# Kernel tuning notes

Hardware: AMD Instinct MI355X
Metric: run time of the kernel (lower is better)

## Reference

```python
import jax, jax.numpy as jnp
import numpy as np


def setup_inputs() -> dict:
    key = jax.random.key(0)
    k1, k2, k3 = jax.random.split(key, 3)
    N, E, D_IN, D_OUT = 100000, 1600000, 64, 64
    x = jax.random.normal(k1, (N, D_IN), dtype=jnp.float32)
    edge_index = jax.random.randint(k2, (2, E), 0, N, dtype=jnp.int64)
    # Glorot-style init for the GCN weight, zero bias (PyG defaults)
    W = jax.random.normal(k3, (D_IN, D_OUT), dtype=jnp.float32) * (1.0 / np.sqrt(D_IN))
    b = jnp.zeros((D_OUT,), dtype=jnp.float32)
    return {"x": x, "edge_index": edge_index, "W": W, "b": b}


def reference(x, edge_index, W, b):
    # GCNConv (PyG semantics, add_self_loops=True, normalize=True) followed by
    # Dropout (eval mode -> identity) and ReLU.
    N = x.shape[0]
    # Linear transform first (small GEMM)
    xw = x @ W  # [N, D_OUT]
    # Add self-loops
    loops = jnp.arange(N, dtype=edge_index.dtype)
    row = jnp.concatenate([edge_index[0], loops])  # source nodes
    col = jnp.concatenate([edge_index[1], loops])  # destination nodes
    # Symmetric degree normalization: deg over destination index (PyG gcn_norm)
    ones = jnp.ones(col.shape[0], dtype=xw.dtype)
    deg = jax.ops.segment_sum(ones, col, num_segments=N)
    deg_inv_sqrt = jnp.where(deg > 0, jax.lax.rsqrt(deg), 0.0)
    norm = deg_inv_sqrt[row] * deg_inv_sqrt[col]  # [E+N]
    # Gather source features, scale, scatter-add to destinations
    msgs = norm[:, None] * xw[row]  # [E+N, D_OUT]
    out = jax.ops.segment_sum(msgs, col, num_segments=N)
    out = out + b
    # dropout in eval mode is identity
    return jax.nn.relu(out)
```

## Files before the change

kernel.cpp:

```cpp
#include <hip/hip_runtime.h>
#include <hip/hip_fp16.h>


#define D 64
#define BW 256
#define CAPB 4800
#define CAPL 6912
#define EPT 16
#define PART_T 512
#define EPB (PART_T * EPT)
#define NBMAX 512
#define GSTRIDE 16

typedef __attribute__((ext_vector_type(8))) short bf16x8;
typedef __attribute__((ext_vector_type(4))) float f32x4;

__device__ __forceinline__ unsigned short f2bf(float f) {
    unsigned u = __float_as_uint(f);
    u += 0x7FFFu + ((u >> 16) & 1u);
    return (unsigned short)(u >> 16);
}

__global__ __launch_bounds__(512)
void k_part(const int* __restrict__ row, const int* __restrict__ col,
            int* __restrict__ gcur, int* __restrict__ dense,
            unsigned short* __restrict__ WT, const float* __restrict__ W,
            unsigned short* __restrict__ xw_h,
            int E, int NBUCK, int N) {
    __shared__ int lh[NBMAX];
    __shared__ int lst[NBMAX + 1];
    __shared__ int bas[NBMAX];
    __shared__ int wsc[8];
    __shared__ int srtv[EPB];
    int tid = threadIdx.x;
    for (int i = tid; i < NBUCK; i += PART_T) lh[i] = 0;
    __syncthreads();
    int e0 = blockIdx.x * EPB + tid;
    int rr[EPT], cc[EPT], pp[EPT];
#pragma unroll
    for (int i = 0; i < EPT; ++i) {
        int e = e0 + i * PART_T;
        if (e < E) {
            cc[i] = __builtin_nontemporal_load(col + e);
            rr[i] = __builtin_nontemporal_load(row + e);
            pp[i] = atomicAdd(&lh[cc[i] >> 8], 1);
        } else {
            cc[i] = -1;
        }
    }
    __syncthreads();
    int rot = (int)((blockIdx.x * 97u) % (unsigned)NBUCK);
    for (int j = tid; j < NBUCK; j += PART_T) {
        int bu = j + rot; if (bu >= NBUCK) bu -= NBUCK;
        int h = lh[bu];
        if (h > 0) bas[bu] = atomicAdd(&gcur[bu * GSTRIDE], h);
    }
    int lane = tid & 63, wv = tid >> 6;
    int v = (tid < NBUCK) ? lh[tid] : 0;
    int inc = v;
#pragma unroll
    for (int o = 1; o < 64; o <<= 1) {
        int u = __shfl_up(inc, o);
        if (lane >= o) inc += u;
    }
    if (lane == 63) wsc[wv] = inc;
    __syncthreads();
    int woff = 0;
#pragma unroll
    for (int w = 0; w < 8; ++w) woff += (w < wv) ? wsc[w] : 0;
    if (tid < NBUCK) lst[tid] = woff + inc - v;
    int tot = min(EPB, E - blockIdx.x * EPB);
    if (tid == 0) lst[NBUCK] = tot;
    __syncthreads();
#pragma unroll
    for (int i = 0; i < EPT; ++i) {
        if (cc[i] >= 0)
            srtv[lst[cc[i] >> 8] + pp[i]] = (rr[i] << 8) | (cc[i] & 255);
    }
    __syncthreads();
    for (int p = tid; p < tot; p += PART_T) {
        int lo = 0, hi = NBUCK;
        while (hi - lo > 1) {
            int mid = (lo + hi) >> 1;
            if (lst[mid] <= p) lo = mid; else hi = mid;
        }
        int gpos = bas[lo] + (p - lst[lo]);
        if (gpos < CAPB) dense[(size_t)lo * CAPB + gpos] = srtv[p];
    }
    if (blockIdx.x == 0) {
        for (int i = tid; i < 4096; i += PART_T) {
            int n = i >> 6, k = i & 63;
            WT[i] = f2bf(W[k * 64 + n]);
        }
        if (tid < 32) ((unsigned*)xw_h)[(size_t)N * 32 + tid] = 0u;
    }
}

__global__ __launch_bounds__(256, 4)
void k_gemm(const float* __restrict__ x, const unsigned short* __restrict__ WT,
            const int* __restrict__ dense, const int* __restrict__ gcur,
            unsigned char* __restrict__ deg8, unsigned short* __restrict__ xw_h,
            int N, int NT) {
    __shared__ int lh[BW];
    int tid = threadIdx.x, b = blockIdx.x;
    lh[tid] = 0;
    __syncthreads();
    int tot = min(gcur[b * GSTRIDE], CAPB);
    const int* dn = dense + (size_t)b * CAPB;
    for (int i = tid; i < tot; i += 256)
        atomicAdd(&lh[__builtin_nontemporal_load(dn + i) & 255], 1);
    __syncthreads();
    {
        int node = b * BW + tid;
        if (node < N) deg8[node] = (unsigned char)min(lh[tid], 255);
    }
    int lane = tid & 63, wv = tid >> 6;
    int m = lane & 15, quad = lane >> 4;
    bf16x8 Bf[4][2];
#pragma unroll
    for (int t = 0; t < 4; ++t)
#pragma unroll
        for (int s = 0; s < 2; ++s)
            Bf[t][s] = *(const bf16x8*)(WT + (t * 16 + m) * 64 + s * 32 + quad * 8);
#pragma unroll
    for (int s = 0; s < 4; ++s) {
        int mt = b * 16 + s * 4 + wv;
        if (mt >= NT) continue;
        int row0 = mt * 16;
        const float* xr = x + (size_t)(row0 + m) * 64 + quad * 8;
        f32x4 a0 = __builtin_nontemporal_load((const f32x4*)(xr));
        f32x4 a1 = __builtin_nontemporal_load((const f32x4*)(xr + 4));
        f32x4 a2 = __builtin_nontemporal_load((const f32x4*)(xr + 32));
        f32x4 a3 = __builtin_nontemporal_load((const f32x4*)(xr + 36));
        bf16x8 A0, A1;
        A0[0] = (short)f2bf(a0[0]); A0[1] = (short)f2bf(a0[1]);
        A0[2] = (short)f2bf(a0[2]); A0[3] = (short)f2bf(a0[3]);
        A0[4] = (short)f2bf(a1[0]); A0[5] = (short)f2bf(a1[1]);
        A0[6] = (short)f2bf(a1[2]); A0[7] = (short)f2bf(a1[3]);
        A1[0] = (short)f2bf(a2[0]); A1[1] = (short)f2bf(a2[1]);
        A1[2] = (short)f2bf(a2[2]); A1[3] = (short)f2bf(a2[3]);
        A1[4] = (short)f2bf(a3[0]); A1[5] = (short)f2bf(a3[1]);
        A1[6] = (short)f2bf(a3[2]); A1[7] = (short)f2bf(a3[3]);
        f32x4 acc[4];
#pragma unroll
        for (int t = 0; t < 4; ++t) {
            acc[t] = (f32x4){0.f, 0.f, 0.f, 0.f};
            acc[t] = __builtin_amdgcn_mfma_f32_16x16x32_bf16(Bf[t][0], A0, acc[t], 0, 0, 0);
            acc[t] = __builtin_amdgcn_mfma_f32_16x16x32_bf16(Bf[t][1], A1, acc[t], 0, 0, 0);
        }
        float dsc = rsqrtf((float)(lh[(row0 + m) & 255] + 1));
        unsigned short* op = xw_h + (size_t)(row0 + m) * 64 + quad * 4;
#pragma unroll
        for (int t = 0; t < 4; ++t) {
            __half2 h0, h1;
            h0.x = __float2half(acc[t][0] * dsc); h0.y = __float2half(acc[t][1] * dsc);
            h1.x = __float2half(acc[t][2] * dsc); h1.y = __float2half(acc[t][3] * dsc);
            uint2 u; u.x = *(unsigned*)&h0; u.y = *(unsigned*)&h1;
            *(uint2*)(op + t * 16) = u;
        }
    }
}

__global__ __launch_bounds__(1024, 8)
void k_gather(const int* __restrict__ dense, const int* __restrict__ gcur,
              const unsigned char* __restrict__ deg8,
              const uint2* __restrict__ xwh, const float* __restrict__ bias,
              float* __restrict__ out, int N) {
    __shared__ int lh[BW], stt[BW], cur[BW];
    __shared__ int wsum[4];
    __shared__ __align__(16) int srtL[CAPL];
    int b = blockIdx.x, tid = threadIdx.x, lane = tid & 63;
    int v = 0, vp = 0, inc = 0;
    if (tid < BW) {
        int node = b * BW + tid;
        v = (node < N) ? (int)deg8[node] : 0;
        lh[tid] = v;
        vp = (v + 15) & ~15; inc = vp;
#pragma unroll
        for (int o = 1; o < 64; o <<= 1) {
            int u = __shfl_up(inc, o);
            if (lane >= o) inc += u;
        }
        if (lane == 63) wsum[tid >> 6] = inc;
    }
    __syncthreads();
    if (tid < BW) {
        int wv4 = tid >> 6, woff = 0;
#pragma unroll
        for (int w = 0; w < 4; ++w) woff += (w < wv4) ? wsum[w] : 0;
        int st = woff + inc - vp;
        stt[tid] = st;
        cur[tid] = st;
    }
    __syncthreads();
    int tot = min(gcur[b * GSTRIDE], CAPB);
    const int* dn = dense + (size_t)b * CAPB;
    for (int i = tid; i < tot; i += 1024) {
        int val = __builtin_nontemporal_load(dn + i);
        int pos = atomicAdd(&cur[val & 255], 1);
        if (pos < CAPL) srtL[pos] = val >> 8;
    }
    __syncthreads();
    if (tid < BW) {
        int e = stt[tid] + v, ep = min(stt[tid] + vp, CAPL);
        for (; e < ep; ++e) srtL[e] = N;
    }
    __syncthreads();
    int q = lane >> 4;
    int l = lane & 15;
    int wv = tid >> 6;
    const float4 bb = ((const float4*)bias)[l];
#define ADDV(h)                                                     \
    {                                                               \
        __half2 h0 = *(__half2*)&(h).x, h1 = *(__half2*)&(h).y;     \
        float2 f0 = __half22float2(h0), f1 = __half22float2(h1);    \
        acc.x += f0.x; acc.y += f0.y; acc.z += f1.x; acc.w += f1.y; \
    }
    for (int nn = wv * 16; nn < wv * 16 + 16; ++nn) {
        int node = b * BW + nn;
        if (node >= N) break;
        int k = lh[nn], s0 = stt[nn];
        int kp = (k + 15) & ~15;
        if (s0 + kp > CAPL) kp = (CAPL > s0) ? ((CAPL - s0) & ~15) : 0;
        float4 acc = make_float4(0.f, 0.f, 0.f, 0.f);
        if (q == 0) { uint2 hs = xwh[(size_t)node * 16 + l]; ADDV(hs); }
        int rounds = kp >> 4;
        if (rounds > 0) {
            int i0 = s0 + q;
            int r0 = srtL[i0], r1 = srtL[i0 + 4], r2 = srtL[i0 + 8], r3 = srtL[i0 + 12];
            uint2 va = xwh[(size_t)r0 * 16 + l];
            uint2 vb = xwh[(size_t)r1 * 16 + l];
            uint2 vc = xwh[(size_t)r2 * 16 + l];
            uint2 vd = xwh[(size_t)r3 * 16 + l];
            for (int r = 1; r < rounds; ++r) {
                i0 += 16;
                int s0n = srtL[i0], s1n = srtL[i0 + 4], s2n = srtL[i0 + 8], s3n = srtL[i0 + 12];
                uint2 wa = xwh[(size_t)s0n * 16 + l];
                uint2 wb = xwh[(size_t)s1n * 16 + l];
                uint2 wc = xwh[(size_t)s2n * 16 + l];
                uint2 wd = xwh[(size_t)s3n * 16 + l];
                ADDV(va); ADDV(vb); ADDV(vc); ADDV(vd);
                va = wa; vb = wb; vc = wc; vd = wd;
            }
            ADDV(va); ADDV(vb); ADDV(vc); ADDV(vd);
        }
        acc.x += __shfl_xor(acc.x, 16); acc.y += __shfl_xor(acc.y, 16);
        acc.z += __shfl_xor(acc.z, 16); acc.w += __shfl_xor(acc.w, 16);
        acc.x += __shfl_xor(acc.x, 32); acc.y += __shfl_xor(acc.y, 32);
        acc.z += __shfl_xor(acc.z, 32); acc.w += __shfl_xor(acc.w, 32);
        if (q == 0) {
            float dn2 = rsqrtf((float)(k + 1));
            f32x4 o;
            o[0] = fmaxf(fmaf(dn2, acc.x, bb.x), 0.f);
            o[1] = fmaxf(fmaf(dn2, acc.y, bb.y), 0.f);
            o[2] = fmaxf(fmaf(dn2, acc.z, bb.z), 0.f);
            o[3] = fmaxf(fmaf(dn2, acc.w, bb.w), 0.f);
            __builtin_nontemporal_store(o, (f32x4*)(out + ((size_t)node * 16 + l) * 4));
        }
    }
#undef ADDV
}

extern "C" void kernel_launch(void* const* d_in, const int* in_sizes, int n_in,
                              void* d_out, int out_size, void* d_ws, size_t ws_size,
                              hipStream_t stream) {
    const float* x    = (const float*)d_in[0];
    const int*   ei   = (const int*)d_in[1];
    const float* W    = (const float*)d_in[2];
    const float* bias = (const float*)d_in[3];
    float* out = (float*)d_out;

    const int N = in_sizes[0] / D;
    const int E = in_sizes[1] / 2;
    const int* row = ei;
    const int* col = ei + E;

    const int NBUCK = (N + BW - 1) / BW;
    const int NB1   = (E + EPB - 1) / EPB;
    const int NT    = (N + 15) / 16;

    char* ws = (char*)d_ws;
    size_t o = 0;
    unsigned short* xw_h = (unsigned short*)(ws + o);
    o += (size_t)(N + 1) * D * sizeof(unsigned short);
    int* dense = (int*)(ws + o); o += (size_t)NBUCK * CAPB * sizeof(int);
    int* gcur  = (int*)(ws + o); o += (size_t)NBUCK * GSTRIDE * sizeof(int);
    unsigned char* deg8 = (unsigned char*)(ws + o); o += (size_t)N;
    o = (o + 15) & ~(size_t)15;
    unsigned short* WT = (unsigned short*)(ws + o); o += 4096 * sizeof(unsigned short);

    hipMemsetAsync(gcur, 0, (size_t)NBUCK * GSTRIDE * sizeof(int), stream);
    k_part<<<NB1, PART_T, 0, stream>>>(row, col, gcur, dense, WT, W, xw_h, E, NBUCK, N);
    k_gemm<<<NBUCK, 256, 0, stream>>>(x, WT, dense, gcur, deg8, xw_h, N, NT);
    k_gather<<<NBUCK, 1024, 0, stream>>>(dense, gcur, deg8, (const uint2*)xw_h,
                                         bias, out, N);
}
```

Baseline: 166.0 us.

## Split buckets into half-blocks, widen gather loads, drop binary search in partition

The gemm and gather kernels now run two blocks per 256-node bucket, each handling 128 nodes. Each half-block filters the bucket's edge list by one bit, which gives twice as many blocks and a smaller LDS footprint. The gather loads 16-byte xw rows with 8 lanes per node instead of 8-byte rows with 16 lanes. The partition kernel stores each sorted edge's bucket id in LDS so it no longer needs a binary search, halves EPT and adds an occupancy hint. The gemm also issues its x loads before the degree count to overlap them, at the cost of each half-block rereading the whole bucket's edge list.

```diff
diff --git a/kernel.cpp b/kernel.cpp
--- a/kernel.cpp
+++ b/kernel.cpp
@@ -5,8 +5,8 @@
 #define D 64
 #define BW 256
 #define CAPB 4800
-#define CAPL 6912
-#define EPT 16
+#define CAPL2 4608
+#define EPT 8
 #define PART_T 512
 #define EPB (PART_T * EPT)
 #define NBMAX 512
@@ -21,7 +21,7 @@
     return (unsigned short)(u >> 16);
 }
 
-__global__ __launch_bounds__(512)
+__global__ __launch_bounds__(512, 4)
 void k_part(const int* __restrict__ row, const int* __restrict__ col,
             int* __restrict__ gcur, int* __restrict__ dense,
             unsigned short* __restrict__ WT, const float* __restrict__ W,
@@ -32,6 +32,7 @@
     __shared__ int bas[NBMAX];
     __shared__ int wsc[8];
     __shared__ int srtv[EPB];
+    __shared__ unsigned short srtb[EPB];
     int tid = threadIdx.x;
     for (int i = tid; i < NBUCK; i += PART_T) lh[i] = 0;
     __syncthreads();
@@ -74,18 +75,18 @@
     __syncthreads();
 #pragma unroll
     for (int i = 0; i < EPT; ++i) {
-        if (cc[i] >= 0)
-            srtv[lst[cc[i] >> 8] + pp[i]] = (rr[i] << 8) | (cc[i] & 255);
+        if (cc[i] >= 0) {
+            int bu = cc[i] >> 8;
+            int pos = lst[bu] + pp[i];
+            srtv[pos] = (rr[i] << 8) | (cc[i] & 255);
+            srtb[pos] = (unsigned short)bu;
+        }
     }
     __syncthreads();
     for (int p = tid; p < tot; p += PART_T) {
-        int lo = 0, hi = NBUCK;
-        while (hi - lo > 1) {
-            int mid = (lo + hi) >> 1;
-            if (lst[mid] <= p) lo = mid; else hi = mid;
-        }
-        int gpos = bas[lo] + (p - lst[lo]);
-        if (gpos < CAPB) dense[(size_t)lo * CAPB + gpos] = srtv[p];
+        int bu = srtb[p];
+        int gpos = bas[bu] + (p - lst[bu]);
+        if (gpos < CAPB) dense[(size_t)bu * CAPB + gpos] = srtv[p];
     }
     if (blockIdx.x == 0) {
         for (int i = tid; i < 4096; i += PART_T) {
@@ -101,21 +102,37 @@
             const int* __restrict__ dense, const int* __restrict__ gcur,
             unsigned char* __restrict__ deg8, unsigned short* __restrict__ xw_h,
             int N, int NT) {
-    __shared__ int lh[BW];
-    int tid = threadIdx.x, b = blockIdx.x;
-    lh[tid] = 0;
-    __syncthreads();
-    int tot = min(gcur[b * GSTRIDE], CAPB);
-    const int* dn = dense + (size_t)b * CAPB;
-    for (int i = tid; i < tot; i += 256)
-        atomicAdd(&lh[__builtin_nontemporal_load(dn + i) & 255], 1);
-    __syncthreads();
-    {
-        int node = b * BW + tid;
-        if (node < N) deg8[node] = (unsigned char)min(lh[tid], 255);
-    }
+    __shared__ int lh[128];
+    int tid = threadIdx.x, b2 = blockIdx.x;
+    int bucket = b2 >> 1, hf = b2 & 1;
     int lane = tid & 63, wv = tid >> 6;
     int m = lane & 15, quad = lane >> 4;
+    f32x4 xa[2][4];
+#pragma unroll
+    for (int s = 0; s < 2; ++s) {
+        int mt = b2 * 8 + s * 4 + wv;
+        if (mt < NT) {
+            const float* xr = x + (size_t)(mt * 16 + m) * 64 + quad * 8;
+            xa[s][0] = __builtin_nontemporal_load((const f32x4*)(xr));
+            xa[s][1] = __builtin_nontemporal_load((const f32x4*)(xr + 4));
+            xa[s][2] = __builtin_nontemporal_load((const f32x4*)(xr + 32));
+            xa[s][3] = __builtin_nontemporal_load((const f32x4*)(xr + 36));
+        }
+    }
+    if (tid < 128) lh[tid] = 0;
+    __syncthreads();
+    int tot = min(gcur[bucket * GSTRIDE], CAPB);
+    const int* dn = dense + (size_t)bucket * CAPB;
+    int hsel = hf << 7;
+    for (int i = tid; i < tot; i += 256) {
+        int val = __builtin_nontemporal_load(dn + i);
+        if ((val & 128) == hsel) atomicAdd(&lh[val & 127], 1);
+    }
+    __syncthreads();
+    if (tid < 128) {
+        int node = b2 * 128 + tid;
+        if (node < N) deg8[node] = (unsigned char)min(lh[tid], 255);
+    }
     bf16x8 Bf[4][2];
 #pragma unroll
     for (int t = 0; t < 4; ++t)
@@ -123,24 +140,19 @@
         for (int s = 0; s < 2; ++s)
             Bf[t][s] = *(const bf16x8*)(WT + (t * 16 + m) * 64 + s * 32 + quad * 8);
 #pragma unroll
-    for (int s = 0; s < 4; ++s) {
-        int mt = b * 16 + s * 4 + wv;
+    for (int s = 0; s < 2; ++s) {
+        int mt = b2 * 8 + s * 4 + wv;
         if (mt >= NT) continue;
         int row0 = mt * 16;
-        const float* xr = x + (size_t)(row0 + m) * 64 + quad * 8;
-        f32x4 a0 = __builtin_nontemporal_load((const f32x4*)(xr));
-        f32x4 a1 = __builtin_nontemporal_load((const f32x4*)(xr + 4));
-        f32x4 a2 = __builtin_nontemporal_load((const f32x4*)(xr + 32));
-        f32x4 a3 = __builtin_nontemporal_load((const f32x4*)(xr + 36));
         bf16x8 A0, A1;
-        A0[0] = (short)f2bf(a0[0]); A0[1] = (short)f2bf(a0[1]);
-        A0[2] = (short)f2bf(a0[2]); A0[3] = (short)f2bf(a0[3]);
-        A0[4] = (short)f2bf(a1[0]); A0[5] = (short)f2bf(a1[1]);
-        A0[6] = (short)f2bf(a1[2]); A0[7] = (short)f2bf(a1[3]);
-        A1[0] = (short)f2bf(a2[0]); A1[1] = (short)f2bf(a2[1]);
-        A1[2] = (short)f2bf(a2[2]); A1[3] = (short)f2bf(a2[3]);
-        A1[4] = (short)f2bf(a3[0]); A1[5] = (short)f2bf(a3[1]);
-        A1[6] = (short)f2bf(a3[2]); A1[7] = (short)f2bf(a3[3]);
+        A0[0] = (short)f2bf(xa[s][0][0]); A0[1] = (short)f2bf(xa[s][0][1]);
+        A0[2] = (short)f2bf(xa[s][0][2]); A0[3] = (short)f2bf(xa[s][0][3]);
+        A0[4] = (short)f2bf(xa[s][1][0]); A0[5] = (short)f2bf(xa[s][1][1]);
+        A0[6] = (short)f2bf(xa[s][1][2]); A0[7] = (short)f2bf(xa[s][1][3]);
+        A1[0] = (short)f2bf(xa[s][2][0]); A1[1] = (short)f2bf(xa[s][2][1]);
+        A1[2] = (short)f2bf(xa[s][2][2]); A1[3] = (short)f2bf(xa[s][2][3]);
+        A1[4] = (short)f2bf(xa[s][3][0]); A1[5] = (short)f2bf(xa[s][3][1]);
+        A1[6] = (short)f2bf(xa[s][3][2]); A1[7] = (short)f2bf(xa[s][3][3]);
         f32x4 acc[4];
 #pragma unroll
         for (int t = 0; t < 4; ++t) {
@@ -148,7 +160,7 @@
             acc[t] = __builtin_amdgcn_mfma_f32_16x16x32_bf16(Bf[t][0], A0, acc[t], 0, 0, 0);
             acc[t] = __builtin_amdgcn_mfma_f32_16x16x32_bf16(Bf[t][1], A1, acc[t], 0, 0, 0);
         }
-        float dsc = rsqrtf((float)(lh[(row0 + m) & 255] + 1));
+        float dsc = rsqrtf((float)(lh[(row0 + m) & 127] + 1));
         unsigned short* op = xw_h + (size_t)(row0 + m) * 64 + quad * 4;
 #pragma unroll
         for (int t = 0; t < 4; ++t) {
@@ -161,18 +173,20 @@
     }
 }
 
-__global__ __launch_bounds__(1024, 8)
+__global__ __launch_bounds__(512, 6)
 void k_gather(const int* __restrict__ dense, const int* __restrict__ gcur,
               const unsigned char* __restrict__ deg8,
-              const uint2* __restrict__ xwh, const float* __restrict__ bias,
+              const uint4* __restrict__ xwh4, const float* __restrict__ bias,
               float* __restrict__ out, int N) {
-    __shared__ int lh[BW], stt[BW], cur[BW];
-    __shared__ int wsum[4];
-    __shared__ __align__(16) int srtL[CAPL];
-    int b = blockIdx.x, tid = threadIdx.x, lane = tid & 63;
+    __shared__ int lh[128], stt[128], cur[128];
+    __shared__ int wsum[2];
+    __shared__ __align__(16) int srtL[CAPL2];
+    int b2 = blockIdx.x, tid = threadIdx.x, lane = tid & 63;
+    int bucket = b2 >> 1, hf = b2 & 1;
+    int nb0 = b2 * 128;
     int v = 0, vp = 0, inc = 0;
-    if (tid < BW) {
-        int node = b * BW + tid;
+    if (tid < 128) {
+        int node = nb0 + tid;
         v = (node < N) ? (int)deg8[node] : 0;
         lh[tid] = v;
         vp = (v + 15) & ~15; inc = vp;
@@ -184,81 +198,91 @@
         if (lane == 63) wsum[tid >> 6] = inc;
     }
     __syncthreads();
-    if (tid < BW) {
-        int wv4 = tid >> 6, woff = 0;
-#pragma unroll
-        for (int w = 0; w < 4; ++w) woff += (w < wv4) ? wsum[w] : 0;
-        int st = woff + inc - vp;
+    if (tid < 128) {
+        int st = inc - vp + ((tid >> 6) ? wsum[0] : 0);
         stt[tid] = st;
         cur[tid] = st;
     }
     __syncthreads();
-    int tot = min(gcur[b * GSTRIDE], CAPB);
-    const int* dn = dense + (size_t)b * CAPB;
-    for (int i = tid; i < tot; i += 1024) {
+    int tot = min(gcur[bucket * GSTRIDE], CAPB);
+    const int* dn = dense + (size_t)bucket * CAPB;
+    int hsel = hf << 7;
+    for (int i = tid; i < tot; i += 512) {
         int val = __builtin_nontemporal_load(dn + i);
-        int pos = atomicAdd(&cur[val & 255], 1);
-        if (pos < CAPL) srtL[pos] = val >> 8;
-    }
-    __syncthreads();
-    if (tid < BW) {
-        int e = stt[tid] + v, ep = min(stt[tid] + vp, CAPL);
+        if ((val & 128) == hsel) {
+            int pos = atomicAdd(&cur[val & 127], 1);
+            if (pos < CAPL2) srtL[pos] = val >> 8;
+        }
+    }
+    __syncthreads();
+    if (tid < 128) {
+        int e = stt[tid] + v, ep = min(stt[tid] + vp, CAPL2);
         for (; e < ep; ++e) srtL[e] = N;
     }
     __syncthreads();
-    int q = lane >> 4;
-    int l = lane & 15;
+    int q = lane >> 3;
+    int l = lane & 7;
     int wv = tid >> 6;
-    const float4 bb = ((const float4*)bias)[l];
-#define ADDV(h)                                                     \
-    {                                                               \
-        __half2 h0 = *(__half2*)&(h).x, h1 = *(__half2*)&(h).y;     \
-        float2 f0 = __half22float2(h0), f1 = __half22float2(h1);    \
-        acc.x += f0.x; acc.y += f0.y; acc.z += f1.x; acc.w += f1.y; \
+    const float4 b0 = ((const float4*)bias)[2 * l];
+    const float4 b1 = ((const float4*)bias)[2 * l + 1];
+#define ADDV16(u)                                                     \
+    {                                                                 \
+        __half2 p0 = *(__half2*)&(u).x, p1 = *(__half2*)&(u).y;       \
+        __half2 p2 = *(__half2*)&(u).z, p3 = *(__half2*)&(u).w;       \
+        float2 f0 = __half22float2(p0), f1 = __half22float2(p1);      \
+        float2 f2 = __half22float2(p2), f3 = __half22float2(p3);      \
+        accA.x += f0.x; accA.y += f0.y; accA.z += f1.x; accA.w += f1.y;\
+        accB.x += f2.x; accB.y += f2.y; accB.z += f3.x; accB.w += f3.y;\
     }
     for (int nn = wv * 16; nn < wv * 16 + 16; ++nn) {
-        int node = b * BW + nn;
+        int node = nb0 + nn;
         if (node >= N) break;
         int k = lh[nn], s0 = stt[nn];
         int kp = (k + 15) & ~15;
-        if (s0 + kp > CAPL) kp = (CAPL > s0) ? ((CAPL - s0) & ~15) : 0;
-        float4 acc = make_float4(0.f, 0.f, 0.f, 0.f);
-        if (q == 0) { uint2 hs = xwh[(size_t)node * 16 + l]; ADDV(hs); }
+        if (s0 + kp > CAPL2) kp = (CAPL2 > s0) ? ((CAPL2 - s0) & ~15) : 0;
+        float4 accA = make_float4(0.f, 0.f, 0.f, 0.f);
+        float4 accB = make_float4(0.f, 0.f, 0.f, 0.f);
+        if (q == 0) { uint4 hs = xwh4[(size_t)node * 8 + l]; ADDV16(hs); }
         int rounds = kp >> 4;
         if (rounds > 0) {
             int i0 = s0 + q;
-            int r0 = srtL[i0], r1 = srtL[i0 + 4], r2 = srtL[i0 + 8], r3 = srtL[i0 + 12];
-            uint2 va = xwh[(size_t)r0 * 16 + l];
-            uint2 vb = xwh[(size_t)r1 * 16 + l];
-            uint2 vc = xwh[(size_t)r2 * 16 + l];
-            uint2 vd = xwh[(size_t)r3 * 16 + l];
+            int r0 = srtL[i0], r1 = srtL[i0 + 8];
+            uint4 va = xwh4[(size_t)r0 * 8 + l];
+            uint4 vb = xwh4[(size_t)r1 * 8 + l];
             for (int r = 1; r < rounds; ++r) {
                 i0 += 16;
-                int s0n = srtL[i0], s1n = srtL[i0 + 4], s2n = srtL[i0 + 8], s3n = srtL[i0 + 12];
-                uint2 wa = xwh[(size_t)s0n * 16 + l];
-                uint2 wb = xwh[(size_t)s1n * 16 + l];
-                uint2 wc = xwh[(size_t)s2n * 16 + l];
-                uint2 wd = xwh[(size_t)s3n * 16 + l];
-                ADDV(va); ADDV(vb); ADDV(vc); ADDV(vd);
-                va = wa; vb = wb; vc = wc; vd = wd;
+                int n0 = srtL[i0], n1 = srtL[i0 + 8];
+                uint4 wa = xwh4[(size_t)n0 * 8 + l];
+                uint4 wb = xwh4[(size_t)n1 * 8 + l];
+                ADDV16(va); ADDV16(vb);
+                va = wa; vb = wb;
             }
-            ADDV(va); ADDV(vb); ADDV(vc); ADDV(vd);
-        }
-        acc.x += __shfl_xor(acc.x, 16); acc.y += __shfl_xor(acc.y, 16);
-        acc.z += __shfl_xor(acc.z, 16); acc.w += __shfl_xor(acc.w, 16);
-        acc.x += __shfl_xor(acc.x, 32); acc.y += __shfl_xor(acc.y, 32);
-        acc.z += __shfl_xor(acc.z, 32); acc.w += __shfl_xor(acc.w, 32);
+            ADDV16(va); ADDV16(vb);
+        }
+#pragma unroll
+        for (int mm = 8; mm < 64; mm <<= 1) {
+            accA.x += __shfl_xor(accA.x, mm); accA.y += __shfl_xor(accA.y, mm);
+            accA.z += __shfl_xor(accA.z, mm); accA.w += __shfl_xor(accA.w, mm);
+            accB.x += __shfl_xor(accB.x, mm); accB.y += __shfl_xor(accB.y, mm);
+            accB.z += __shfl_xor(accB.z, mm); accB.w += __shfl_xor(accB.w, mm);
+        }
         if (q == 0) {
             float dn2 = rsqrtf((float)(k + 1));
-            f32x4 o;
-            o[0] = fmaxf(fmaf(dn2, acc.x, bb.x), 0.f);
-            o[1] = fmaxf(fmaf(dn2, acc.y, bb.y), 0.f);
-            o[2] = fmaxf(fmaf(dn2, acc.z, bb.z), 0.f);
-            o[3] = fmaxf(fmaf(dn2, acc.w, bb.w), 0.f);
-            __builtin_nontemporal_store(o, (f32x4*)(out + ((size_t)node * 16 + l) * 4));
-        }
-    }
-#undef ADDV
+            f32x4 o1, o2;
+            o1[0] = fmaxf(fmaf(dn2, accA.x, b0.x), 0.f);
+            o1[1] = fmaxf(fmaf(dn2, accA.y, b0.y), 0.f);
+            o1[2] = fmaxf(fmaf(dn2, accA.z, b0.z), 0.f);
+            o1[3] = fmaxf(fmaf(dn2, accA.w, b0.w), 0.f);
+            o2[0] = fmaxf(fmaf(dn2, accB.x, b1.x), 0.f);
+            o2[1] = fmaxf(fmaf(dn2, accB.y, b1.y), 0.f);
+            o2[2] = fmaxf(fmaf(dn2, accB.z, b1.z), 0.f);
+            o2[3] = fmaxf(fmaf(dn2, accB.w, b1.w), 0.f);
+            float* op = out + (size_t)node * 64 + l * 8;
+            __builtin_nontemporal_store(o1, (f32x4*)op);
+            __builtin_nontemporal_store(o2, (f32x4*)(op + 4));
+        }
+    }
+#undef ADDV16
 }
 
 extern "C" void kernel_launch(void* const* d_in, const int* in_sizes, int n_in,
@@ -278,6 +302,7 @@
     const int NBUCK = (N + BW - 1) / BW;
     const int NB1   = (E + EPB - 1) / EPB;
     const int NT    = (N + 15) / 16;
+    const int NH    = 2 * NBUCK;
 
     char* ws = (char*)d_ws;
     size_t o = 0;
@@ -291,7 +316,7 @@
 
     hipMemsetAsync(gcur, 0, (size_t)NBUCK * GSTRIDE * sizeof(int), stream);
     k_part<<<NB1, PART_T, 0, stream>>>(row, col, gcur, dense, WT, W, xw_h, E, NBUCK, N);
-    k_gemm<<<NBUCK, 256, 0, stream>>>(x, WT, dense, gcur, deg8, xw_h, N, NT);
-    k_gather<<<NBUCK, 1024, 0, stream>>>(dense, gcur, deg8, (const uint2*)xw_h,
-                                         bias, out, N);
-}
+    k_gemm<<<NH, 256, 0, stream>>>(x, WT, dense, gcur, deg8, xw_h, N, NT);
+    k_gather<<<NH, 512, 0, stream>>>(dense, gcur, deg8, (const uint4*)xw_h,
+                                     bias, out, N);
+}
```

After: 169.2 us. Within noise of the previous version (+1.9%).
